# Kernel optimization log

Measured on AMD Instinct MI355X. Metric: run time of the kernel, lower is better.

## Reference

```python
import jax, jax.numpy as jnp
import numpy as np

CH = 512
GROUPS = 32  # _valid_num_groups(512, 32)
EPS = 1e-6

def setup_inputs() -> dict:
    key = jax.random.key(0)
    ks = jax.random.split(key, 11)
    B, C, H, W = 8, CH, 64, 64
    s = 0.02
    return {
        "x": jax.random.normal(ks[0], (B, C, H, W), jnp.float32),
        "gn_w": jnp.ones((C,), jnp.float32),
        "gn_b": jnp.zeros((C,), jnp.float32),
        "q_w": jax.random.normal(ks[1], (C, C), jnp.float32) * s,
        "q_b": jnp.zeros((C,), jnp.float32),
        "k_w": jax.random.normal(ks[2], (C, C), jnp.float32) * s,
        "k_b": jnp.zeros((C,), jnp.float32),
        "v_w": jax.random.normal(ks[3], (C, C), jnp.float32) * s,
        "v_b": jnp.zeros((C,), jnp.float32),
        "proj_w": jax.random.normal(ks[4], (C, C), jnp.float32) * s,
        "proj_b": jnp.zeros((C,), jnp.float32),
    }

def _group_norm(x, w, b):
    B, C, H, W = x.shape
    g = GROUPS
    xg = x.reshape(B, g, C // g, H, W)
    mu = xg.mean(axis=(2, 3, 4), keepdims=True)
    var = xg.var(axis=(2, 3, 4), keepdims=True)
    xn = ((xg - mu) * jax.lax.rsqrt(var + EPS)).reshape(B, C, H, W)
    return xn * w[None, :, None, None] + b[None, :, None, None]

def _conv1x1(h, w, b):
    # h: [B,C,H,W]; w: [Cout,Cin]; 1x1 conv == channel matmul
    return jnp.einsum('bchw,dc->bdhw', h, w) + b[None, :, None, None]

def reference(x, gn_w, gn_b, q_w, q_b, k_w, k_b, v_w, v_b, proj_w, proj_b):
    B, C, H, W = x.shape
    N = H * W
    h = _group_norm(x, gn_w, gn_b)
    q = _conv1x1(h, q_w, q_b).reshape(B, C, N)  # [B,C,N]
    k = _conv1x1(h, k_w, k_b).reshape(B, C, N)
    v = _conv1x1(h, v_w, v_b).reshape(B, C, N)
    # attn[b,i,j] = sum_c q[b,c,i]*k[b,c,j] scaled
    attn = jnp.einsum('bci,bcj->bij', q, k) * (C ** -0.5)
    attn = jax.nn.softmax(attn, axis=-1)
    # out[b,c,i] = sum_j v[b,c,j]*attn[b,i,j]  (bmm(v, attn^T))
    o = jnp.einsum('bcj,bij->bci', v, attn).reshape(B, C, H, W)
    o = _conv1x1(o, proj_w, proj_b)
    return x + o
```

## Files before the change

### kernel.cpp

```cpp
#include <hip/hip_runtime.h>

typedef unsigned short u16;
typedef __attribute__((ext_vector_type(8))) short short8;
typedef __attribute__((ext_vector_type(4))) float f32x4;

__device__ __forceinline__ u16 f32_to_bf16(float f) {
  unsigned u = __float_as_uint(f);
  u += 0x7fffu + ((u >> 16) & 1u);
  return (u16)(u >> 16);
}
__device__ __forceinline__ float bf16_to_f32(u16 h) {
  return __uint_as_float(((unsigned)h) << 16);
}

#define GLD_LDS16(gp, lp)                                                  \
  __builtin_amdgcn_global_load_lds(                                        \
      (const __attribute__((address_space(1))) void*)(gp),                 \
      (__attribute__((address_space(3))) void*)(lp), 16, 0, 0)

#define WAITVM(n) asm volatile("s_waitcnt vmcnt(" #n ")" ::: "memory")

__device__ __forceinline__ void wg_barrier() {
  asm volatile("" ::: "memory");
  __builtin_amdgcn_s_barrier();
  asm volatile("" ::: "memory");
}

__global__ __launch_bounds__(256) void cvt4_f32_bf16(const float* __restrict__ s0,
                                                     const float* __restrict__ s1,
                                                     const float* __restrict__ s2,
                                                     const float* __restrict__ s3,
                                                     u16* __restrict__ d0,
                                                     u16* __restrict__ d1,
                                                     u16* __restrict__ d2,
                                                     u16* __restrict__ d3) {
  const float* s = blockIdx.y == 0 ? s0 : blockIdx.y == 1 ? s1 : blockIdx.y == 2 ? s2 : s3;
  u16* d = blockIdx.y == 0 ? d0 : blockIdx.y == 1 ? d1 : blockIdx.y == 2 ? d2 : d3;
  int i = blockIdx.x * 256 + threadIdx.x;
  float4 v = ((const float4*)s)[i];
  uint2 r;
  r.x = (unsigned)f32_to_bf16(v.x) | ((unsigned)f32_to_bf16(v.y) << 16);
  r.y = (unsigned)f32_to_bf16(v.z) | ((unsigned)f32_to_bf16(v.w) << 16);
  ((uint2*)d)[i] = r;
}

__global__ __launch_bounds__(1024) void gn_stats(const float* __restrict__ x,
                                                 float2* __restrict__ stats) {
  int bg = blockIdx.x;
  const float* xp = x + (long)bg * 65536;
  int t = threadIdx.x;
  float s = 0.f, ss = 0.f;
  for (int i = t; i < 16384; i += 1024) {
    float4 v = ((const float4*)xp)[i];
    s += (v.x + v.y) + (v.z + v.w);
    ss += (v.x * v.x + v.y * v.y) + (v.z * v.z + v.w * v.w);
  }
#pragma unroll
  for (int o = 32; o; o >>= 1) { s += __shfl_xor(s, o); ss += __shfl_xor(ss, o); }
  __shared__ float rs[16], rq[16];
  int wave = t >> 6, lane = t & 63;
  if (lane == 0) { rs[wave] = s; rq[wave] = ss; }
  __syncthreads();
  if (wave == 0) {
    float a = lane < 16 ? rs[lane] : 0.f;
    float b = lane < 16 ? rq[lane] : 0.f;
#pragma unroll
    for (int o = 8; o; o >>= 1) { a += __shfl_xor(a, o); b += __shfl_xor(b, o); }
    if (lane == 0) {
      float mean = a * (1.f / 65536.f);
      float var = b * (1.f / 65536.f) - mean * mean;
      stats[bg] = make_float2(mean, rsqrtf(var + 1e-6f));
    }
  }
}

__global__ __launch_bounds__(256) void gn_apply_t(const float* __restrict__ x,
                                                  const float* __restrict__ gw,
                                                  const float* __restrict__ gb,
                                                  const float2* __restrict__ stats,
                                                  u16* __restrict__ hT) {
  const int g = blockIdx.y, bb = blockIdx.z;
  const float2 st = stats[bb * 32 + g];
  const float mean = st.x, rstd = st.y;
  const float* xp = x + ((long)bb * 512 + g * 16) * 4096;
  u16* hp = hT + (long)bb * 4096 * 512 + g * 16;
  const int i = blockIdx.x * 1024 + threadIdx.x * 4;
#pragma unroll
  for (int half = 0; half < 2; ++half) {
    float w[8], bv[8];
#pragma unroll
    for (int c = 0; c < 8; ++c) {
      w[c] = gw[g * 16 + half * 8 + c] * rstd;
      bv[c] = gb[g * 16 + half * 8 + c];
    }
    float v[8][4];
#pragma unroll
    for (int c = 0; c < 8; ++c) {
      float4 f = *(const float4*)(xp + (long)(half * 8 + c) * 4096 + i);
      v[c][0] = f.x; v[c][1] = f.y; v[c][2] = f.z; v[c][3] = f.w;
    }
#pragma unroll
    for (int p = 0; p < 4; ++p) {
      u16 o[8];
#pragma unroll
      for (int c = 0; c < 8; ++c) o[c] = f32_to_bf16((v[c][p] - mean) * w[c] + bv[c]);
      *(int4*)(hp + (long)(i + p) * 512 + half * 8) = *(int4*)o;
    }
  }
}

template <int BN, int MODE, int SWZ>
__global__ __launch_bounds__(512, MODE == 2 ? 4 : 2) void gemm256(
    const u16* __restrict__ Ab, long sA, int lda,
    const u16* __restrict__ Bb, long sB, int ldb,
    u16* __restrict__ Cb, long sC, int ldc,
    const float* __restrict__ biasM, const float* __restrict__ biasN,
    float scale, int K,
    float* __restrict__ psum, const float* __restrict__ SinvP) {
  constexpr int NFR = BN / 64;
  constexpr int BCH = (BN * 32 * 2) / (512 * 16);
  constexpr int DEPTH = (MODE == 2 ? 3 : 4);
  constexpr int AHEAD = DEPTH - 1;
  __shared__ __align__(16) u16 As[DEPTH][256 * 32];
  __shared__ __align__(16) u16 Bs[DEPTH][BN * 32];
  const u16* A = Ab + (long)blockIdx.z * sA;
  const u16* B = Bb + (long)blockIdx.z * sB;

  int bx = blockIdx.x, by = blockIdx.y;
  if (SWZ == 1) {
    const int id = blockIdx.x + gridDim.x * blockIdx.y;
    const int c = id & 7, s = id >> 3;
    bx = s % gridDim.x;
    by = 2 * c + s / gridDim.x;
  } else if (SWZ == 2) {
    const int id = blockIdx.x + (blockIdx.y << 4);
    const int c = id & 7, s = id >> 3;
    bx = ((c & 1) << 3) + (s & 7);
    by = ((c >> 1) << 2) + (s >> 3);
  }

  const int m0 = by * 256, n0 = bx * BN;
  const int t = threadIdx.x;
  const int wave = t >> 6, lane = t & 63;
  const int wy = wave >> 2, wx = wave & 3;
  const int lr = lane & 15, q = lane >> 4;
  const int NT = K >> 5;

  long aoff[2];
  int aldsb[2];
#pragma unroll
  for (int cc = 0; cc < 2; ++cc) {
    int c = cc * 512 + t;
    int row = c >> 2, sl = c & 3;
    int qs = sl ^ ((row >> 1) & 3);
    aoff[cc] = (long)(m0 + row) * lda + qs * 8;
    aldsb[cc] = (cc * 512 + wave * 64) * 8;
  }
  long boff[BCH];
  int bldsb[BCH];
#pragma unroll
  for (int cc = 0; cc < BCH; ++cc) {
    int c = cc * 512 + t;
    int row = c >> 2, sl = c & 3;
    int qs = sl ^ ((row >> 1) & 3);
    boff[cc] = (long)(n0 + row) * ldb + qs * 8;
    bldsb[cc] = (cc * 512 + wave * 64) * 8;
  }

  auto stageA = [&](int tt2, int buf) {
    const long kk = (long)tt2 << 5;
#pragma unroll
    for (int cc = 0; cc < 2; ++cc) GLD_LDS16(A + aoff[cc] + kk, &As[buf][aldsb[cc]]);
  };
  auto stageB = [&](int tt2, int buf) {
    const long kk = (long)tt2 << 5;
#pragma unroll
    for (int cc = 0; cc < BCH; ++cc) GLD_LDS16(B + boff[cc] + kk, &Bs[buf][bldsb[cc]]);
  };

  const int so = ((q ^ ((lr >> 1) & 3)) << 3);
  const int arow = wy * 128;
  const int brow = wx * (BN / 4);

  f32x4 acc[8][NFR] = {};

#pragma unroll
  for (int pt = 0; pt < AHEAD; ++pt) { stageA(pt, pt); stageB(pt, pt); }

  int bcur = 0;
  for (int tt = 0; tt < NT; ++tt) {
    const int bst = (bcur == 0) ? DEPTH - 1 : bcur - 1;
    if (tt + AHEAD < NT) stageA(tt + AHEAD, bst);
    const int nf = NT - 1 - tt;
    if (MODE == 2) {
      if (nf >= 2) WAITVM(5);
      else if (nf == 1) WAITVM(3);
      else WAITVM(0);
    } else {
      if (nf >= 3) WAITVM(10);
      else if (nf == 2) WAITVM(8);
      else if (nf == 1) WAITVM(4);
      else WAITVM(0);
    }
    wg_barrier();
    short8 a0[4], bfr[NFR];
#pragma unroll
    for (int i = 0; i < 4; ++i)
      a0[i] = *(const short8*)(&As[bcur][0] + (arow + i * 16 + lr) * 32 + so);
#pragma unroll
    for (int j = 0; j < NFR; ++j)
      bfr[j] = *(const short8*)(&Bs[bcur][0] + (brow + j * 16 + lr) * 32 + so);
    __builtin_amdgcn_s_setprio(1);
#pragma unroll
    for (int i = 0; i < 4; ++i)
#pragma unroll
      for (int j = 0; j < NFR; ++j)
        acc[i][j] = __builtin_amdgcn_mfma_f32_16x16x32_bf16(a0[i], bfr[j], acc[i][j], 0, 0, 0);
    __builtin_amdgcn_s_setprio(0);
    wg_barrier();
    if (tt + AHEAD < NT) stageB(tt + AHEAD, bst);
    short8 a1[4];
#pragma unroll
    for (int i = 0; i < 4; ++i)
      a1[i] = *(const short8*)(&As[bcur][0] + (arow + 64 + i * 16 + lr) * 32 + so);
    __builtin_amdgcn_s_setprio(1);
#pragma unroll
    for (int i = 0; i < 4; ++i)
#pragma unroll
      for (int j = 0; j < NFR; ++j)
        acc[4 + i][j] = __builtin_amdgcn_mfma_f32_16x16x32_bf16(a1[i], bfr[j], acc[4 + i][j], 0, 0, 0);
    __builtin_amdgcn_s_setprio(0);
    wg_barrier();
    bcur = (bcur + 1 == DEPTH) ? 0 : bcur + 1;
  }

  if (MODE == 1) {
    float* sred = (float*)&As[0][0];
#pragma unroll
    for (int i = 0; i < 8; ++i) {
#pragma unroll
      for (int r = 0; r < 4; ++r) {
        const int mr = m0 + wy * 128 + i * 16 + q * 4 + r;
        float s = 0.f;
#pragma unroll
        for (int j = 0; j < NFR; ++j) {
          const int nc = n0 + wx * 64 + j * 16 + lr;
          float p = __expf(acc[i][j][r]);
          s += p;
          Cb[(long)blockIdx.z * sC + (long)mr * ldc + nc] = f32_to_bf16(p);
        }
#pragma unroll
        for (int o = 1; o < 16; o <<= 1) s += __shfl_xor(s, o);
        if (lr == 0) sred[wx * 256 + wy * 128 + i * 16 + q * 4 + r] = s;
      }
    }
    __syncthreads();
    if (wx == 0 && lr == 0) {
#pragma unroll
      for (int i = 0; i < 8; ++i)
#pragma unroll
        for (int r = 0; r < 4; ++r) {
          const int row = wy * 128 + i * 16 + q * 4 + r;
          const float S = sred[row] + sred[256 + row] + sred[512 + row] + sred[768 + row];
          psum[((long)blockIdx.z * 16 + bx) * 4096 + (m0 + row)] = S;
        }
    }
    return;
  }

#pragma unroll
  for (int i = 0; i < 8; ++i) {
#pragma unroll
    for (int r = 0; r < 4; ++r) {
      const int mr = m0 + wy * 128 + i * 16 + q * 4 + r;
      float rowmul = 1.f, rowadd = 0.f;
      if (MODE == 2) rowmul = SinvP[(long)blockIdx.z * 4096 + mr];
      else if (biasM) rowadd = biasM[mr];
#pragma unroll
      for (int j = 0; j < NFR; ++j) {
        const int nc = n0 + wx * (BN / 4) + j * 16 + lr;
        float vv = acc[i][j][r];
        if (MODE == 2) {
          vv *= rowmul;
        } else {
          vv += rowadd;
          if (biasN) vv += biasN[nc];
          vv *= scale;
        }
        Cb[(long)blockIdx.z * sC + (long)mr * ldc + nc] = f32_to_bf16(vv);
      }
    }
  }
}

__global__ __launch_bounds__(256) void combine_sums(const float* __restrict__ ps,
                                                    float* __restrict__ Sinv) {
  const int row = blockIdx.x * 256 + threadIdx.x;
  const long z = blockIdx.y;
  const float* p = ps + z * 16 * 4096 + row;
  float s = 0.f;
#pragma unroll
  for (int i = 0; i < 16; ++i) s += p[(long)i * 4096];
  Sinv[z * 4096 + row] = 1.0f / s;
}

template <int EPI>
__global__ __launch_bounds__(256) void gemm128(
    const u16* __restrict__ Ab, long sA, int lda,
    const u16* __restrict__ Bb, long sB, int ldb,
    void* __restrict__ Cb, long sC, int ldc,
    const float* __restrict__ biasM, const float* __restrict__ biasN,
    float scale, const float* __restrict__ res, long sR, int K) {
  const u16* A = Ab + (long)blockIdx.z * sA;
  const u16* B = Bb + (long)blockIdx.z * sB;
  const int m0 = blockIdx.y * 128, n0 = blockIdx.x * 128;
  const int t = threadIdx.x;
  const int wave = t >> 6, lane = t & 63;
  const int wy = wave >> 1, wx = wave & 1;
  const int lr = lane & 15, q = lane >> 4;
  __shared__ __align__(16) u16 As[128 * 32];
  __shared__ __align__(16) u16 Bs[128 * 32];
  f32x4 acc[4][4] = {};
  for (int k0 = 0; k0 < K; k0 += 32) {
#pragma unroll
    for (int c = 0; c < 2; ++c) {
      const int chunk = c * 256 + t;
      const int row = chunk >> 2, ko = (chunk & 3) << 3;
      const int ldsoff = (c * 256 + wave * 64) * 8;
      GLD_LDS16(A + (long)(m0 + row) * lda + (k0 + ko), As + ldsoff);
      GLD_LDS16(B + (long)(n0 + row) * ldb + (k0 + ko), Bs + ldsoff);
    }
    __syncthreads();
    short8 af[4], bf[4];
#pragma unroll
    for (int i = 0; i < 4; ++i)
      af[i] = *(const short8*)(&As[(wy * 64 + i * 16 + lr) * 32 + q * 8]);
#pragma unroll
    for (int j = 0; j < 4; ++j)
      bf[j] = *(const short8*)(&Bs[(wx * 64 + j * 16 + lr) * 32 + q * 8]);
#pragma unroll
    for (int i = 0; i < 4; ++i)
#pragma unroll
      for (int j = 0; j < 4; ++j)
        acc[i][j] = __builtin_amdgcn_mfma_f32_16x16x32_bf16(af[i], bf[j], acc[i][j], 0, 0, 0);
    __syncthreads();
  }
#pragma unroll
  for (int i = 0; i < 4; ++i) {
#pragma unroll
    for (int r = 0; r < 4; ++r) {
      const int mr = m0 + wy * 64 + i * 16 + q * 4 + r;
      const float bm = biasM ? biasM[mr] : 0.f;
#pragma unroll
      for (int j = 0; j < 4; ++j) {
        const int nc = n0 + wx * 64 + j * 16 + lr;
        float vv = acc[i][j][r] + bm;
        if (biasN) vv += biasN[nc];
        vv *= scale;
        const long off = (long)blockIdx.z * sC + (long)mr * ldc + nc;
        if (EPI == 0) {
          ((u16*)Cb)[off] = f32_to_bf16(vv);
        } else {
          ((float*)Cb)[off] = vv + res[(long)blockIdx.z * sR + (long)mr * ldc + nc];
        }
      }
    }
  }
}

extern "C" void kernel_launch(void* const* d_in, const int* in_sizes, int n_in,
                              void* d_out, int out_size, void* d_ws, size_t ws_size,
                              hipStream_t stream) {
  const float* x = (const float*)d_in[0];
  const float* gn_w = (const float*)d_in[1];
  const float* gn_b = (const float*)d_in[2];
  const float* q_w = (const float*)d_in[3];
  const float* q_b = (const float*)d_in[4];
  const float* k_w = (const float*)d_in[5];
  const float* k_b = (const float*)d_in[6];
  const float* v_w = (const float*)d_in[7];
  const float* v_b = (const float*)d_in[8];
  const float* p_w = (const float*)d_in[9];
  const float* p_b = (const float*)d_in[10];

  char* ws = (char*)d_ws;
  const size_t MB = 1ull << 20;
  u16* wqb = (u16*)(ws + 0);
  u16* wkb = (u16*)(ws + 512 * 1024);
  u16* wvb = (u16*)(ws + 1 * MB);
  u16* wpb = (u16*)(ws + 3 * MB / 2);
  u16* hb = (u16*)(ws + 2 * MB);
  u16* vb = (u16*)(ws + 34 * MB);
  u16* Pb = (u16*)(ws + 66 * MB);
  float2* gnstats = (float2*)(ws + 66 * MB);
  u16* qb = (u16*)d_out;
  u16* kb = (u16*)d_out + 512L * 4096 * 8;
  u16* ob = hb;

  int NB = 1;
  if (ws_size >= (66 + 8 * 32 + 5) * MB) NB = 8;
  else if (ws_size >= (66 + 4 * 32 + 5) * MB) NB = 4;
  else if (ws_size >= (66 + 2 * 32 + 5) * MB) NB = 2;

  float* psum = (float*)(ws + 66 * MB + (size_t)NB * 32 * MB);
  float* Si = psum + (size_t)NB * 16 * 4096;

  cvt4_f32_bf16<<<dim3(256, 4), 256, 0, stream>>>(q_w, k_w, v_w, p_w, wqb, wkb, wvb, wpb);
  gn_stats<<<256, 1024, 0, stream>>>(x, gnstats);
  gn_apply_t<<<dim3(4, 32, 8), 256, 0, stream>>>(x, gn_w, gn_b, gnstats, hb);

  const long sCN = 512L * 4096;
  const long sNN = 4096L * 4096;
  const float scale = 0.04419417382415922f;

  gemm256<256, 0, 1><<<dim3(2, 16, 8), 512, 0, stream>>>(
      hb, sCN, 512, wqb, 0, 512, qb, sCN, 512, nullptr, q_b, scale, 512,
      nullptr, nullptr);
  gemm256<256, 0, 1><<<dim3(2, 16, 8), 512, 0, stream>>>(
      hb, sCN, 512, wkb, 0, 512, kb, sCN, 512, nullptr, k_b, 1.0f, 512,
      nullptr, nullptr);
  gemm256<256, 0, 0><<<dim3(16, 2, 8), 512, 0, stream>>>(
      wvb, 0, 512, hb, sCN, 512, vb, sCN, 4096, v_b, nullptr, 1.0f, 512,
      nullptr, nullptr);

  for (int b0 = 0; b0 < 8; b0 += NB) {
    gemm256<256, 1, 2><<<dim3(16, 16, NB), 512, 0, stream>>>(
        qb + b0 * sCN, sCN, 512, kb + b0 * sCN, sCN, 512, Pb, sNN, 4096,
        nullptr, nullptr, 1.0f, 512, psum, nullptr);
    combine_sums<<<dim3(16, NB), 256, 0, stream>>>(psum, Si);
    gemm256<128, 2, 1><<<dim3(4, 16, NB), 512, 0, stream>>>(
        Pb, sNN, 4096, vb + b0 * sCN, sCN, 4096, ob + b0 * sCN, sCN, 512,
        nullptr, nullptr, 1.0f, 4096, nullptr, Si);
  }

  gemm128<1><<<dim3(32, 4, 8), 256, 0, stream>>>(
      wpb, 0, 512, ob, sCN, 512, (float*)d_out, sCN, 4096, p_b, nullptr, 1.0f,
      x, sCN, 512);
}
```

Measured before the change: 861.4 us.

## Double the GEMM K-tile to 64 and merge A/B staging into one pipeline stage

Raises the K step per iteration from 32 to 64, with a wider 8-slot XOR swizzle, and stages A and B together in one batch of async global-to-LDS loads. The pipeline depth becomes 3 for BN=128 and 2 otherwise, with matching vmcnt waits. The mid-iteration barrier is removed, so there are half as many K iterations and barriers. The trade-off is more LDS per block, fewer stages in flight, and a uniform launch bound of 2 occupancy in place of 4 for MODE 2, which may reduce latency hiding.

```diff
diff --git a/kernel.cpp b/kernel.cpp
--- a/kernel.cpp
+++ b/kernel.cpp
@@ -110,7 +110,7 @@
 }
 
 template <int BN, int MODE, int SWZ>
-__global__ __launch_bounds__(512, MODE == 2 ? 4 : 2) void gemm256(
+__global__ __launch_bounds__(512, 2) void gemm256(
     const u16* __restrict__ Ab, long sA, int lda,
     const u16* __restrict__ Bb, long sB, int ldb,
     u16* __restrict__ Cb, long sC, int ldc,
@@ -118,11 +118,13 @@
     float scale, int K,
     float* __restrict__ psum, const float* __restrict__ SinvP) {
   constexpr int NFR = BN / 64;
-  constexpr int BCH = (BN * 32 * 2) / (512 * 16);
-  constexpr int DEPTH = (MODE == 2 ? 3 : 4);
+  constexpr int ACH = 4;
+  constexpr int BCH = (BN * 64 * 2) / (512 * 16);
+  constexpr int DEPTH = (BN == 128 ? 3 : 2);
   constexpr int AHEAD = DEPTH - 1;
-  __shared__ __align__(16) u16 As[DEPTH][256 * 32];
-  __shared__ __align__(16) u16 Bs[DEPTH][BN * 32];
+  constexpr int L = ACH + BCH;
+  __shared__ __align__(16) u16 As[DEPTH][256 * 64];
+  __shared__ __align__(16) u16 Bs[DEPTH][BN * 64];
   const u16* A = Ab + (long)blockIdx.z * sA;
   const u16* B = Bb + (long)blockIdx.z * sB;
 
@@ -144,15 +146,15 @@
   const int wave = t >> 6, lane = t & 63;
   const int wy = wave >> 2, wx = wave & 3;
   const int lr = lane & 15, q = lane >> 4;
-  const int NT = K >> 5;
-
-  long aoff[2];
-  int aldsb[2];
-#pragma unroll
-  for (int cc = 0; cc < 2; ++cc) {
+  const int NT = K >> 6;
+
+  long aoff[ACH];
+  int aldsb[ACH];
+#pragma unroll
+  for (int cc = 0; cc < ACH; ++cc) {
     int c = cc * 512 + t;
-    int row = c >> 2, sl = c & 3;
-    int qs = sl ^ ((row >> 1) & 3);
+    int row = c >> 3, sl = c & 7;
+    int qs = sl ^ (row & 7);
     aoff[cc] = (long)(m0 + row) * lda + qs * 8;
     aldsb[cc] = (cc * 512 + wave * 64) * 8;
   }
@@ -161,75 +163,72 @@
 #pragma unroll
   for (int cc = 0; cc < BCH; ++cc) {
     int c = cc * 512 + t;
-    int row = c >> 2, sl = c & 3;
-    int qs = sl ^ ((row >> 1) & 3);
+    int row = c >> 3, sl = c & 7;
+    int qs = sl ^ (row & 7);
     boff[cc] = (long)(n0 + row) * ldb + qs * 8;
     bldsb[cc] = (cc * 512 + wave * 64) * 8;
   }
 
-  auto stageA = [&](int tt2, int buf) {
-    const long kk = (long)tt2 << 5;
-#pragma unroll
-    for (int cc = 0; cc < 2; ++cc) GLD_LDS16(A + aoff[cc] + kk, &As[buf][aldsb[cc]]);
-  };
-  auto stageB = [&](int tt2, int buf) {
-    const long kk = (long)tt2 << 5;
+  auto stageAB = [&](int tt2, int buf) {
+    const long kk = (long)tt2 << 6;
+#pragma unroll
+    for (int cc = 0; cc < ACH; ++cc) GLD_LDS16(A + aoff[cc] + kk, &As[buf][aldsb[cc]]);
 #pragma unroll
     for (int cc = 0; cc < BCH; ++cc) GLD_LDS16(B + boff[cc] + kk, &Bs[buf][bldsb[cc]]);
   };
 
-  const int so = ((q ^ ((lr >> 1) & 3)) << 3);
+  const int so0 = ((q ^ (lr & 7)) << 3);
+  const int so1 = (((4 + q) ^ (lr & 7)) << 3);
   const int arow = wy * 128;
   const int brow = wx * (BN / 4);
 
   f32x4 acc[8][NFR] = {};
 
 #pragma unroll
-  for (int pt = 0; pt < AHEAD; ++pt) { stageA(pt, pt); stageB(pt, pt); }
+  for (int pt = 0; pt < AHEAD; ++pt) stageAB(pt, pt);
 
   int bcur = 0;
   for (int tt = 0; tt < NT; ++tt) {
-    const int bst = (bcur == 0) ? DEPTH - 1 : bcur - 1;
-    if (tt + AHEAD < NT) stageA(tt + AHEAD, bst);
+    const int bst = (bcur + AHEAD >= DEPTH) ? bcur + AHEAD - DEPTH : bcur + AHEAD;
+    if (tt + AHEAD < NT) stageAB(tt + AHEAD, bst);
     const int nf = NT - 1 - tt;
-    if (MODE == 2) {
-      if (nf >= 2) WAITVM(5);
-      else if (nf == 1) WAITVM(3);
+    if constexpr (DEPTH == 3) {
+      if (nf >= 2) WAITVM(12);
+      else if (nf == 1) WAITVM(6);
       else WAITVM(0);
     } else {
-      if (nf >= 3) WAITVM(10);
-      else if (nf == 2) WAITVM(8);
-      else if (nf == 1) WAITVM(4);
+      if (nf >= 1) WAITVM(8);
       else WAITVM(0);
     }
     wg_barrier();
-    short8 a0[4], bfr[NFR];
-#pragma unroll
-    for (int i = 0; i < 4; ++i)
-      a0[i] = *(const short8*)(&As[bcur][0] + (arow + i * 16 + lr) * 32 + so);
-#pragma unroll
-    for (int j = 0; j < NFR; ++j)
-      bfr[j] = *(const short8*)(&Bs[bcur][0] + (brow + j * 16 + lr) * 32 + so);
-    __builtin_amdgcn_s_setprio(1);
-#pragma unroll
-    for (int i = 0; i < 4; ++i)
+    const u16* Ab_ = &As[bcur][0];
+    const u16* Bb_ = &Bs[bcur][0];
+#pragma unroll
+    for (int h = 0; h < 2; ++h) {
+      const int so = h ? so1 : so0;
+      short8 bfr[NFR], a0[4], a1[4];
 #pragma unroll
       for (int j = 0; j < NFR; ++j)
-        acc[i][j] = __builtin_amdgcn_mfma_f32_16x16x32_bf16(a0[i], bfr[j], acc[i][j], 0, 0, 0);
-    __builtin_amdgcn_s_setprio(0);
-    wg_barrier();
-    if (tt + AHEAD < NT) stageB(tt + AHEAD, bst);
-    short8 a1[4];
-#pragma unroll
-    for (int i = 0; i < 4; ++i)
-      a1[i] = *(const short8*)(&As[bcur][0] + (arow + 64 + i * 16 + lr) * 32 + so);
-    __builtin_amdgcn_s_setprio(1);
-#pragma unroll
-    for (int i = 0; i < 4; ++i)
-#pragma unroll
-      for (int j = 0; j < NFR; ++j)
-        acc[4 + i][j] = __builtin_amdgcn_mfma_f32_16x16x32_bf16(a1[i], bfr[j], acc[4 + i][j], 0, 0, 0);
-    __builtin_amdgcn_s_setprio(0);
+        bfr[j] = *(const short8*)(Bb_ + (brow + j * 16 + lr) * 64 + so);
+#pragma unroll
+      for (int i = 0; i < 4; ++i)
+        a0[i] = *(const short8*)(Ab_ + (arow + i * 16 + lr) * 64 + so);
+#pragma unroll
+      for (int i = 0; i < 4; ++i)
+        a1[i] = *(const short8*)(Ab_ + (arow + 64 + i * 16 + lr) * 64 + so);
+      __builtin_amdgcn_s_setprio(1);
+#pragma unroll
+      for (int i = 0; i < 4; ++i)
+#pragma unroll
+        for (int j = 0; j < NFR; ++j)
+          acc[i][j] = __builtin_amdgcn_mfma_f32_16x16x32_bf16(a0[i], bfr[j], acc[i][j], 0, 0, 0);
+#pragma unroll
+      for (int i = 0; i < 4; ++i)
+#pragma unroll
+        for (int j = 0; j < NFR; ++j)
+          acc[4 + i][j] = __builtin_amdgcn_mfma_f32_16x16x32_bf16(a1[i], bfr[j], acc[4 + i][j], 0, 0, 0);
+      __builtin_amdgcn_s_setprio(0);
+    }
     wg_barrier();
     bcur = (bcur + 1 == DEPTH) ? 0 : bcur + 1;
   }
```

New measurement: 828.8 us. 3.8% less time.
